# Kernel tuning notes

Hardware: AMD Instinct MI355X
Metric: run time of the kernel (lower is better)

## Reference

```python
import jax, jax.numpy as jnp
import numpy as np

N_NODES = 100000
N_EDGES = 1600000
IN_DIM = 64
OUT_DIM = 64
K_HEADS = 4
HEAD_DIM = OUT_DIM // K_HEADS


def setup_inputs() -> dict:
    key = jax.random.key(0)
    ks = jax.random.split(key, 12)
    x = jax.random.normal(ks[0], (N_NODES, IN_DIM), dtype=jnp.float32)
    edge_index = jax.random.randint(ks[1], (2, N_EDGES), 0, N_NODES, dtype=jnp.int64)
    edge_sign = jax.random.randint(ks[2], (N_EDGES,), 0, 2, dtype=jnp.int64)
    s = 1.0 / np.sqrt(IN_DIM)
    Wl_w = jax.random.uniform(ks[3], (OUT_DIM, IN_DIM), minval=-s, maxval=s, dtype=jnp.float32)
    Wl_b = jax.random.uniform(ks[4], (OUT_DIM,), minval=-s, maxval=s, dtype=jnp.float32)
    sign_tab = jax.random.normal(ks[5], (2, HEAD_DIM), dtype=jnp.float32)
    so = 1.0 / np.sqrt(OUT_DIM)
    Wh_w = jax.random.uniform(ks[6], (OUT_DIM, OUT_DIM), minval=-so, maxval=so, dtype=jnp.float32)
    Wh_b = jax.random.uniform(ks[7], (OUT_DIM,), minval=-so, maxval=so, dtype=jnp.float32)
    mlp_w1 = jax.random.uniform(ks[8], (OUT_DIM, OUT_DIM), minval=-so, maxval=so, dtype=jnp.float32)
    mlp_b1 = jax.random.uniform(ks[9], (OUT_DIM,), minval=-so, maxval=so, dtype=jnp.float32)
    mlp_w2 = jax.random.uniform(ks[10], (OUT_DIM, OUT_DIM), minval=-so, maxval=so, dtype=jnp.float32)
    mlp_b2 = jax.random.uniform(ks[11], (OUT_DIM,), minval=-so, maxval=so, dtype=jnp.float32)
    eps = jnp.zeros((1,), dtype=jnp.float32)
    return {"x": x, "edge_index": edge_index, "edge_sign": edge_sign,
            "Wl_w": Wl_w, "Wl_b": Wl_b, "sign_tab": sign_tab,
            "Wh_w": Wh_w, "Wh_b": Wh_b, "mlp_w1": mlp_w1, "mlp_b1": mlp_b1,
            "mlp_w2": mlp_w2, "mlp_b2": mlp_b2, "eps": eps}


def reference(x, edge_index, edge_sign, Wl_w, Wl_b, sign_tab, Wh_w, Wh_b,
              mlp_w1, mlp_b1, mlp_w2, mlp_b2, eps):
    N = x.shape[0]
    row, col = edge_index[0], edge_index[1]
    h = x @ Wl_w.T + Wl_b                              # [N, out_dim]
    hr = h.reshape(N, K_HEADS, HEAD_DIM)               # [N, K, hd]
    h_i = hr[row]                                      # [E, K, hd]
    h_j = hr[col]                                      # [E, K, hd]
    s_emb = sign_tab[edge_sign][:, None, :]            # [E, 1, hd]
    score = jnp.sum(h_i * h_j * s_emb, axis=-1)        # [E, K]
    # segment softmax over edges grouped by target node (row)
    mx = jax.ops.segment_max(score, row, num_segments=N)
    mx = jnp.where(jnp.isfinite(mx), mx, 0.0)          # empty segments -> 0
    ex = jnp.exp(score - mx[row])                      # [E, K]
    den = jax.ops.segment_sum(ex, row, num_segments=N)
    alpha = ex / (den[row] + 1e-16)                    # [E, K]
    # scatter-add weighted messages per head (vectorized over heads)
    msg = h_j * alpha[:, :, None]                      # [E, K, hd]
    aggr = jax.ops.segment_sum(msg, row, num_segments=N)  # [N, K, hd]
    m_l = aggr.reshape(N, OUT_DIM) @ Wh_w.T + Wh_b
    z = (1.0 + eps) * h + m_l
    hid = jax.nn.relu(z @ mlp_w1.T + mlp_b1)
    return hid @ mlp_w2.T + mlp_b2
```

## Files before the change

kernel.cpp:

```cpp
#include <hip/hip_runtime.h>

#define DIM 64
#define NBUCK 256
#define BSHIFT 9
#define BCAP 12288
#define CHUNK 4096

typedef __attribute__((ext_vector_type(4))) float f32x4;
typedef __attribute__((ext_vector_type(8))) short short8;
typedef __attribute__((ext_vector_type(4))) unsigned short ushort4v;

#define MFMA16(a, b, c) __builtin_amdgcn_mfma_f32_16x16x32_bf16(a, b, c, 0, 0, 0)

template <int CTRL>
__device__ __forceinline__ float qperm(float v) {
    return __int_as_float(__builtin_amdgcn_update_dpp(
        0, __float_as_int(v), CTRL, 0xF, 0xF, true));
}

__device__ __forceinline__ void cvt8(const float* f, short8& hi, short8& lo) {
#pragma unroll
    for (int e = 0; e < 8; ++e) {
        const unsigned u = __float_as_uint(f[e]);
        hi[e] = (short)(u >> 16);
        const float hf = __uint_as_float(u & 0xFFFF0000u);
        lo[e] = (short)(__float_as_uint(f[e] - hf) >> 16);
    }
}

__device__ __forceinline__ unsigned short bf16rne(float f) {
    const unsigned u = __float_as_uint(f);
    return (unsigned short)((u + 0x7FFFu + ((u >> 16) & 1u)) >> 16);
}

__global__ __launch_bounds__(256) void prep_kernel(
    const float* __restrict__ Wl, const float* __restrict__ Wh,
    const float* __restrict__ W1, const float* __restrict__ W2,
    short8* __restrict__ wf)
{
    const int tid = threadIdx.x;
    const int m = tid >> 6, l = tid & 63;
    const float* W = (m == 0) ? Wl : (m == 1) ? Wh : (m == 2) ? W1 : W2;
    const int o = l & 15;
    const int kg = (l >> 4) * 8;
#pragma unroll
    for (int t = 0; t < 4; ++t)
#pragma unroll
        for (int s = 0; s < 2; ++s) {
            float f[8];
#pragma unroll
            for (int e = 0; e < 8; ++e)
                f[e] = W[(o + 16 * t) * DIM + 32 * s + kg + e];
            short8 hi, lo;
            cvt8(f, hi, lo);
            const int base = (((m * 4 + t) * 2 + s) * 2);
            wf[(base + 0) * 64 + l] = hi;
            wf[(base + 1) * 64 + l] = lo;
        }
}

__global__ __launch_bounds__(256, 3) void gemm64_kernel(
    const float* __restrict__ x, const short8* __restrict__ wf,
    const float* __restrict__ bias, float* __restrict__ h,
    unsigned short* __restrict__ hb, int N)
{
    const int l = threadIdx.x & 63;
    const int gw = blockIdx.x * 4 + (threadIdx.x >> 6);
    const int nw = gridDim.x * 4;
    const int nstrips = (N + 15) >> 4;
    const int lr = l & 15, lk = (l >> 4) * 8, lrow4 = (l >> 4) * 4;

    short8 wh_[4][2], wl_[4][2];
#pragma unroll
    for (int t = 0; t < 4; ++t)
#pragma unroll
        for (int s = 0; s < 2; ++s) {
            wh_[t][s] = wf[(((0 * 4 + t) * 2 + s) * 2 + 0) * 64 + l];
            wl_[t][s] = wf[(((0 * 4 + t) * 2 + s) * 2 + 1) * 64 + l];
        }
    float b4[4];
#pragma unroll
    for (int t = 0; t < 4; ++t) b4[t] = bias[lr + 16 * t];

    for (int strip = gw; strip < nstrips; strip += nw) {
        const int rbase = strip * 16;
        const int arow = min(rbase + lr, N - 1);
        short8 ah[2], al[2];
#pragma unroll
        for (int s = 0; s < 2; ++s) {
            const float4 p0 = *reinterpret_cast<const float4*>(x + (size_t)arow * DIM + 32 * s + lk);
            const float4 p1 = *reinterpret_cast<const float4*>(x + (size_t)arow * DIM + 32 * s + lk + 4);
            float f[8] = {p0.x, p0.y, p0.z, p0.w, p1.x, p1.y, p1.z, p1.w};
            cvt8(f, ah[s], al[s]);
        }
        f32x4 acc[4];
#pragma unroll
        for (int t = 0; t < 4; ++t) acc[t] = (f32x4){b4[t], b4[t], b4[t], b4[t]};
#pragma unroll
        for (int s = 0; s < 2; ++s) {
#pragma unroll
            for (int t = 0; t < 4; ++t) acc[t] = MFMA16(ah[s], wh_[t][s], acc[t]);
#pragma unroll
            for (int t = 0; t < 4; ++t) acc[t] = MFMA16(ah[s], wl_[t][s], acc[t]);
#pragma unroll
            for (int t = 0; t < 4; ++t) acc[t] = MFMA16(al[s], wh_[t][s], acc[t]);
        }
#pragma unroll
        for (int t = 0; t < 4; ++t)
#pragma unroll
            for (int rg = 0; rg < 4; ++rg) {
                const int row = rbase + lrow4 + rg;
                if (row < N) {
                    h[(size_t)row * DIM + lr + 16 * t] = acc[t][rg];
                    hb[(size_t)row * DIM + lr + 16 * t] = bf16rne(acc[t][rg]);
                }
            }
    }
}

__global__ __launch_bounds__(256, 2) void tail_kernel(
    const float* __restrict__ aggr, const float* __restrict__ hres,
    const short8* __restrict__ wf,
    const float* __restrict__ bh, const float* __restrict__ b1,
    const float* __restrict__ b2, const float* __restrict__ eps,
    float* __restrict__ out, int N)
{
    __shared__ float zb[4][16 * 68];
    const int l = threadIdx.x & 63;
    const int w = threadIdx.x >> 6;
    const int gw = blockIdx.x * 4 + w;
    const int nw = gridDim.x * 4;
    const int nstrips = (N + 15) >> 4;
    const int lr = l & 15, lk = (l >> 4) * 8, lrow4 = (l >> 4) * 4;
    float* zw = zb[w];

    short8 whh[4][2], w1h[4][2], w2h[4][2];
#pragma unroll
    for (int t = 0; t < 4; ++t)
#pragma unroll
        for (int s = 0; s < 2; ++s) {
            whh[t][s] = wf[(((1 * 4 + t) * 2 + s) * 2 + 0) * 64 + l];
            w1h[t][s] = wf[(((2 * 4 + t) * 2 + s) * 2 + 0) * 64 + l];
            w2h[t][s] = wf[(((3 * 4 + t) * 2 + s) * 2 + 0) * 64 + l];
        }
    float bh4[4], b14[4], b24[4];
#pragma unroll
    for (int t = 0; t < 4; ++t) {
        bh4[t] = bh[lr + 16 * t];
        b14[t] = b1[lr + 16 * t];
        b24[t] = b2[lr + 16 * t];
    }
    const float escale = 1.0f + eps[0];

    for (int strip = gw; strip < nstrips; strip += nw) {
        const int rbase = strip * 16;

        float vh[4][4];
#pragma unroll
        for (int t = 0; t < 4; ++t)
#pragma unroll
            for (int rg = 0; rg < 4; ++rg)
                vh[t][rg] = hres[(size_t)min(rbase + lrow4 + rg, N - 1) * DIM + lr + 16 * t];

        const int arow = min(rbase + lr, N - 1);
        short8 ah[2], al[2];
#pragma unroll
        for (int s = 0; s < 2; ++s) {
            const float4 p0 = *reinterpret_cast<const float4*>(aggr + (size_t)arow * DIM + 32 * s + lk);
            const float4 p1 = *reinterpret_cast<const float4*>(aggr + (size_t)arow * DIM + 32 * s + lk + 4);
            float f[8] = {p0.x, p0.y, p0.z, p0.w, p1.x, p1.y, p1.z, p1.w};
            cvt8(f, ah[s], al[s]);
        }
        short8 lo_[4][2];
#pragma unroll
        for (int t = 0; t < 4; ++t)
#pragma unroll
            for (int s = 0; s < 2; ++s)
                lo_[t][s] = wf[(((1 * 4 + t) * 2 + s) * 2 + 1) * 64 + l];
        f32x4 acc[4];
#pragma unroll
        for (int t = 0; t < 4; ++t) acc[t] = (f32x4){bh4[t], bh4[t], bh4[t], bh4[t]};
#pragma unroll
        for (int s = 0; s < 2; ++s) {
#pragma unroll
            for (int t = 0; t < 4; ++t) acc[t] = MFMA16(ah[s], whh[t][s], acc[t]);
#pragma unroll
            for (int t = 0; t < 4; ++t) acc[t] = MFMA16(ah[s], lo_[t][s], acc[t]);
#pragma unroll
            for (int t = 0; t < 4; ++t) acc[t] = MFMA16(al[s], whh[t][s], acc[t]);
        }
#pragma unroll
        for (int t = 0; t < 4; ++t)
#pragma unroll
            for (int rg = 0; rg < 4; ++rg)
                zw[(lrow4 + rg) * 68 + lr + 16 * t] = fmaf(escale, vh[t][rg], acc[t][rg]);
        asm volatile("s_waitcnt lgkmcnt(0)" ::: "memory");

        short8 zh[2], zl[2];
#pragma unroll
        for (int s = 0; s < 2; ++s) {
            const float4 q0 = *reinterpret_cast<const float4*>(zw + lr * 68 + 32 * s + lk);
            const float4 q1 = *reinterpret_cast<const float4*>(zw + lr * 68 + 32 * s + lk + 4);
            float f[8] = {q0.x, q0.y, q0.z, q0.w, q1.x, q1.y, q1.z, q1.w};
            cvt8(f, zh[s], zl[s]);
        }
#pragma unroll
        for (int t = 0; t < 4; ++t)
#pragma unroll
            for (int s = 0; s < 2; ++s)
                lo_[t][s] = wf[(((2 * 4 + t) * 2 + s) * 2 + 1) * 64 + l];
#pragma unroll
        for (int t = 0; t < 4; ++t) acc[t] = (f32x4){b14[t], b14[t], b14[t], b14[t]};
#pragma unroll
        for (int s = 0; s < 2; ++s) {
#pragma unroll
            for (int t = 0; t < 4; ++t) acc[t] = MFMA16(zh[s], w1h[t][s], acc[t]);
#pragma unroll
            for (int t = 0; t < 4; ++t) acc[t] = MFMA16(zh[s], lo_[t][s], acc[t]);
#pragma unroll
            for (int t = 0; t < 4; ++t) acc[t] = MFMA16(zl[s], w1h[t][s], acc[t]);
        }
#pragma unroll
        for (int t = 0; t < 4; ++t)
#pragma unroll
            for (int rg = 0; rg < 4; ++rg)
                zw[(lrow4 + rg) * 68 + lr + 16 * t] = fmaxf(acc[t][rg], 0.f);
        asm volatile("s_waitcnt lgkmcnt(0)" ::: "memory");

        short8 hh[2], hl[2];
#pragma unroll
        for (int s = 0; s < 2; ++s) {
            const float4 q0 = *reinterpret_cast<const float4*>(zw + lr * 68 + 32 * s + lk);
            const float4 q1 = *reinterpret_cast<const float4*>(zw + lr * 68 + 32 * s + lk + 4);
            float f[8] = {q0.x, q0.y, q0.z, q0.w, q1.x, q1.y, q1.z, q1.w};
            cvt8(f, hh[s], hl[s]);
        }
#pragma unroll
        for (int t = 0; t < 4; ++t)
#pragma unroll
            for (int s = 0; s < 2; ++s)
                lo_[t][s] = wf[(((3 * 4 + t) * 2 + s) * 2 + 1) * 64 + l];
#pragma unroll
        for (int t = 0; t < 4; ++t) acc[t] = (f32x4){b24[t], b24[t], b24[t], b24[t]};
#pragma unroll
        for (int s = 0; s < 2; ++s) {
#pragma unroll
            for (int t = 0; t < 4; ++t) acc[t] = MFMA16(hh[s], w2h[t][s], acc[t]);
#pragma unroll
            for (int t = 0; t < 4; ++t) acc[t] = MFMA16(hh[s], lo_[t][s], acc[t]);
#pragma unroll
            for (int t = 0; t < 4; ++t) acc[t] = MFMA16(hl[s], w2h[t][s], acc[t]);
        }
#pragma unroll
        for (int t = 0; t < 4; ++t)
#pragma unroll
            for (int rg = 0; rg < 4; ++rg) {
                const int row = rbase + lrow4 + rg;
                if (row < N) out[(size_t)row * DIM + lr + 16 * t] = acc[t][rg];
            }
    }
}

__global__ __launch_bounds__(256) void zero256_kernel(int* __restrict__ p) {
    p[threadIdx.x] = 0;
}

__device__ __forceinline__ int wave_incl_scan(int v, int lane) {
#pragma unroll
    for (int off = 1; off < 64; off <<= 1) {
        int t = __shfl_up(v, (unsigned)off, 64);
        if (lane >= off) v += t;
    }
    return v;
}

__global__ __launch_bounds__(256) void bin_kernel(
    const int* __restrict__ ei, const int* __restrict__ sgn,
    int* __restrict__ bcursor, int* __restrict__ records, int E)
{
    const int tid = threadIdx.x;
    const int base = blockIdx.x * CHUNK;
    __shared__ int lcnt[NBUCK];
    __shared__ int lbase[NBUCK];
    lcnt[tid] = 0;
    __syncthreads();
    const int lim = min(CHUNK, E - base);
    for (int k = tid; k < lim; k += 256)
        atomicAdd(&lcnt[ei[base + k] >> BSHIFT], 1);
    __syncthreads();
    const int c = lcnt[tid];
    lbase[tid] = c ? atomicAdd(&bcursor[tid], c) : 0;
    lcnt[tid] = 0;
    __syncthreads();
    for (int k = tid; k < lim; k += 256) {
        const int e = base + k;
        const int r  = ei[e];
        const int cc = ei[E + e];
        const int s  = sgn[e];
        const int b  = r >> BSHIFT;
        const int idx = lbase[b] + atomicAdd(&lcnt[b], 1);
        if (idx < BCAP)
            records[b * BCAP + idx] = cc | (s << 17) | ((r & 511) << 18);
    }
}

__global__ __launch_bounds__(256) void scan256_kernel(
    const int* __restrict__ bcursor, int* __restrict__ csrb,
    int* __restrict__ offsets, int* __restrict__ edata, int N, int E)
{
    const int tid = threadIdx.x, lane = tid & 63, w = tid >> 6;
    const int v = min(bcursor[tid], BCAP);
    const int inc = wave_incl_scan(v, lane);
    __shared__ int wtot[4];
    if (lane == 63) wtot[w] = inc;
    __syncthreads();
    int add = 0;
#pragma unroll
    for (int i = 0; i < 4; ++i)
        if (i < w) add += wtot[i];
    csrb[tid] = add + inc - v;
    if (tid == 0) { offsets[N] = E; edata[E] = 0; }
}

__global__ __launch_bounds__(256) void build_kernel(
    const int* __restrict__ records, const int* __restrict__ bcursor,
    const int* __restrict__ csrb, int* __restrict__ offsets,
    int* __restrict__ edata, int N)
{
    const int b = blockIdx.x;
    const int tid = threadIdx.x, lane = tid & 63, w = tid >> 6;
    const int nbase = b << BSHIFT;
    const int nn = min(512, N - nbase);
    if (nn <= 0) return;
    const int cnt = min(bcursor[b], BCAP);
    const int base_csr = csrb[b];
    const int* rec = records + b * BCAP;

    __shared__ int ncnt[512];
    __shared__ int wtot[8];
    __shared__ int stag[BCAP];

    ncnt[tid] = 0; ncnt[256 + tid] = 0;
    __syncthreads();
    for (int i = tid; i < cnt; i += 256)
        atomicAdd(&ncnt[rec[i] >> 18], 1);
    __syncthreads();
    const int v0 = ncnt[tid], v1 = ncnt[256 + tid];
    const int i0 = wave_incl_scan(v0, lane);
    if (lane == 63) wtot[w] = i0;
    const int i1 = wave_incl_scan(v1, lane);
    if (lane == 63) wtot[4 + w] = i1;
    __syncthreads();
    int a0 = 0, a1 = 0;
#pragma unroll
    for (int i = 0; i < 4; ++i) {
        if (i < w) { a0 += wtot[i]; a1 += wtot[4 + i]; }
    }
    const int half = wtot[0] + wtot[1] + wtot[2] + wtot[3];
    const int e0 = a0 + i0 - v0;
    const int e1 = half + a1 + i1 - v1;
    if (tid < nn)       offsets[nbase + tid]       = base_csr + e0;
    if (256 + tid < nn) offsets[nbase + 256 + tid] = base_csr + e1;
    __syncthreads();
    ncnt[tid] = e0; ncnt[256 + tid] = e1;
    __syncthreads();
    for (int i = tid; i < cnt; i += 256) {
        const int rcd = rec[i];
        const int p = atomicAdd(&ncnt[rcd >> 18], 1);
        stag[p] = (rcd & 0x1FFFF) | (((rcd >> 17) & 1) << 20);
    }
    __syncthreads();
    for (int i = tid; i < cnt; i += 256)
        edata[base_csr + i] = stag[i];
}

__global__ __launch_bounds__(256) void attn_kernel(
    const float* __restrict__ h, const unsigned short* __restrict__ hb,
    const int* __restrict__ offsets, const int* __restrict__ edata,
    const float* __restrict__ sign_tab, float* __restrict__ aggr, int n)
{
    const int lane = threadIdx.x & 63;
    const int gl   = lane & 15;
    const int node = blockIdx.x * 16 + ((threadIdx.x >> 6) << 2) + (lane >> 4);
    const bool alive = node < n;

    int beg = 0, deg = 0;
    if (alive) {
        beg = offsets[node];
        deg = offsets[node + 1] - beg;
    }
    float4 hi = make_float4(0.f, 0.f, 0.f, 0.f);
    if (alive) hi = *reinterpret_cast<const float4*>(h + (size_t)node * DIM + gl * 4);

    const float4 s0 = *reinterpret_cast<const float4*>(sign_tab + (gl & 3) * 4);
    const float4 s1 = *reinterpret_cast<const float4*>(sign_tab + 16 + (gl & 3) * 4);
    const float4 hs0 = make_float4(hi.x * s0.x, hi.y * s0.y, hi.z * s0.z, hi.w * s0.w);
    const float4 hs1 = make_float4(hi.x * s1.x, hi.y * s1.y, hi.z * s1.z, hi.w * s1.w);

    const int degm1 = deg - 1;
    int maxdeg = max(deg, __shfl_xor(deg, 16, 64));
    maxdeg = max(maxdeg, __shfl_xor(maxdeg, 32, 64));

    float den = 0.f;
    float4 msg = make_float4(0.f, 0.f, 0.f, 0.f);

    for (int e = 0; e < maxdeg; e += 4) {
        int idx[4], pk[4];
#pragma unroll
        for (int u = 0; u < 4; ++u) idx[u] = max(0, min(e + u, degm1));
#pragma unroll
        for (int u = 0; u < 4; ++u) pk[u] = edata[beg + idx[u]];

        float4 hj[4];
#pragma unroll
        for (int u = 0; u < 4; ++u) {
            const int col = pk[u] & 0xFFFFF;
            const ushort4v v = *reinterpret_cast<const ushort4v*>(hb + (size_t)col * DIM + gl * 4);
            hj[u].x = __uint_as_float(((unsigned)v.x) << 16);
            hj[u].y = __uint_as_float(((unsigned)v.y) << 16);
            hj[u].z = __uint_as_float(((unsigned)v.z) << 16);
            hj[u].w = __uint_as_float(((unsigned)v.w) << 16);
        }

        float sc[4];
#pragma unroll
        for (int u = 0; u < 4; ++u) {
            const float4 wv = (pk[u] >> 20) ? hs1 : hs0;
            float s = wv.x * hj[u].x;
            s = fmaf(wv.y, hj[u].y, s);
            s = fmaf(wv.z, hj[u].z, s);
            s = fmaf(wv.w, hj[u].w, s);
            sc[u] = s;
        }
#pragma unroll
        for (int u = 0; u < 4; ++u) sc[u] += qperm<0xB1>(sc[u]);
#pragma unroll
        for (int u = 0; u < 4; ++u) sc[u] += qperm<0x4E>(sc[u]);

#pragma unroll
        for (int u = 0; u < 4; ++u) {
            const float ex = (e + u < deg) ? __expf(sc[u]) : 0.f;
            den += ex;
            msg.x = fmaf(ex, hj[u].x, msg.x);
            msg.y = fmaf(ex, hj[u].y, msg.y);
            msg.z = fmaf(ex, hj[u].z, msg.z);
            msg.w = fmaf(ex, hj[u].w, msg.w);
        }
    }

    if (alive) {
        const float inv = 1.0f / (den + 1e-16f);
        float4 o = make_float4(msg.x * inv, msg.y * inv, msg.z * inv, msg.w * inv);
        *reinterpret_cast<float4*>(aggr + (size_t)node * DIM + gl * 4) = o;
    }
}

extern "C" void kernel_launch(void* const* d_in, const int* in_sizes, int n_in,
                              void* d_out, int out_size, void* d_ws, size_t ws_size,
                              hipStream_t stream) {
    const float* x        = (const float*)d_in[0];
    const int*   ei       = (const int*)d_in[1];
    const int*   esign    = (const int*)d_in[2];
    const float* Wl_w     = (const float*)d_in[3];
    const float* Wl_b     = (const float*)d_in[4];
    const float* sign_tab = (const float*)d_in[5];
    const float* Wh_w     = (const float*)d_in[6];
    const float* Wh_b     = (const float*)d_in[7];
    const float* w1       = (const float*)d_in[8];
    const float* b1       = (const float*)d_in[9];
    const float* w2       = (const float*)d_in[10];
    const float* b2       = (const float*)d_in[11];
    const float* eps      = (const float*)d_in[12];
    float* out = (float*)d_out;

    const int N = in_sizes[0] / DIM;
    const int E = in_sizes[2];

    float* h       = (float*)d_ws;
    float* aggr    = h + (size_t)N * DIM;
    int*   records = (int*)aggr;
    int*   edata   = (int*)(aggr + (size_t)N * DIM);
    int*   bcursor = edata + (E + 1);
    int*   csrb    = bcursor + NBUCK;
    int*   offsets = csrb + NBUCK;
    short8* wf     = (short8*)(offsets + ((N + 1 + 3) & ~3));
    unsigned short* hb = (unsigned short*)d_out;

    prep_kernel<<<1, 256, 0, stream>>>(Wl_w, Wh_w, w1, w2, wf);

    gemm64_kernel<<<512, 256, 0, stream>>>(x, wf, Wl_b, h, hb, N);

    zero256_kernel<<<1, 256, 0, stream>>>(bcursor);
    bin_kernel<<<(E + CHUNK - 1) / CHUNK, 256, 0, stream>>>(ei, esign, bcursor, records, E);
    scan256_kernel<<<1, 256, 0, stream>>>(bcursor, csrb, offsets, edata, N, E);
    build_kernel<<<NBUCK, 256, 0, stream>>>(records, bcursor, csrb, offsets, edata, N);

    attn_kernel<<<(N + 15) / 16, 256, 0, stream>>>(h, hb, offsets, edata, sign_tab, aggr, N);

    tail_kernel<<<512, 256, 0, stream>>>(aggr, h, wf, Wh_b, b1, b2, eps, out, N);
}
```

Baseline: 132.9 us.

## Vectorize edge binning loads and streamline attention gather with packed math

The bin kernel now loads eight row, column and sign values per thread with int4 vector loads, using a smaller chunk so each block holds exactly 2048 edges. The attention kernel drops the per-edge index clamping by zero-padding edata past E, which lets the loop read beyond a node's degree safely. It also uses 32-bit address arithmetic, nontemporal edge loads and packed float2 math for the score and message accumulation. Together these cut instruction count and memory transactions, but they rely on the padding being large enough for the maximum over-read and on 32-bit offsets not overflowing.

```diff
diff --git a/kernel.cpp b/kernel.cpp
--- a/kernel.cpp
+++ b/kernel.cpp
@@ -4,11 +4,11 @@
 #define NBUCK 256
 #define BSHIFT 9
 #define BCAP 12288
-#define CHUNK 4096
+#define CHUNK 2048
 
 typedef __attribute__((ext_vector_type(4))) float f32x4;
+typedef __attribute__((ext_vector_type(2))) float f32x2v;
 typedef __attribute__((ext_vector_type(8))) short short8;
-typedef __attribute__((ext_vector_type(4))) unsigned short ushort4v;
 
 #define MFMA16(a, b, c) __builtin_amdgcn_mfma_f32_16x16x32_bf16(a, b, c, 0, 0, 0)
 
@@ -285,22 +285,57 @@
     lcnt[tid] = 0;
     __syncthreads();
     const int lim = min(CHUNK, E - base);
-    for (int k = tid; k < lim; k += 256)
-        atomicAdd(&lcnt[ei[base + k] >> BSHIFT], 1);
-    __syncthreads();
-    const int c = lcnt[tid];
-    lbase[tid] = c ? atomicAdd(&bcursor[tid], c) : 0;
-    lcnt[tid] = 0;
-    __syncthreads();
-    for (int k = tid; k < lim; k += 256) {
-        const int e = base + k;
-        const int r  = ei[e];
-        const int cc = ei[E + e];
-        const int s  = sgn[e];
-        const int b  = r >> BSHIFT;
-        const int idx = lbase[b] + atomicAdd(&lcnt[b], 1);
-        if (idx < BCAP)
-            records[b * BCAP + idx] = cc | (s << 17) | ((r & 511) << 18);
+    if (lim == CHUNK && (E & 3) == 0) {
+        int r[8];
+        {
+            const int4 a = *(reinterpret_cast<const int4*>(ei + base) + tid * 2);
+            const int4 b = *(reinterpret_cast<const int4*>(ei + base) + tid * 2 + 1);
+            r[0]=a.x; r[1]=a.y; r[2]=a.z; r[3]=a.w;
+            r[4]=b.x; r[5]=b.y; r[6]=b.z; r[7]=b.w;
+        }
+#pragma unroll
+        for (int i = 0; i < 8; ++i) atomicAdd(&lcnt[r[i] >> BSHIFT], 1);
+        __syncthreads();
+        const int c = lcnt[tid];
+        lbase[tid] = c ? atomicAdd(&bcursor[tid], c) : 0;
+        lcnt[tid] = 0;
+        __syncthreads();
+        int cc[8], ss[8];
+        {
+            const int4 a = *(reinterpret_cast<const int4*>(ei + E + base) + tid * 2);
+            const int4 b = *(reinterpret_cast<const int4*>(ei + E + base) + tid * 2 + 1);
+            cc[0]=a.x; cc[1]=a.y; cc[2]=a.z; cc[3]=a.w;
+            cc[4]=b.x; cc[5]=b.y; cc[6]=b.z; cc[7]=b.w;
+            const int4 s2 = *(reinterpret_cast<const int4*>(sgn + base) + tid * 2);
+            const int4 s3 = *(reinterpret_cast<const int4*>(sgn + base) + tid * 2 + 1);
+            ss[0]=s2.x; ss[1]=s2.y; ss[2]=s2.z; ss[3]=s2.w;
+            ss[4]=s3.x; ss[5]=s3.y; ss[6]=s3.z; ss[7]=s3.w;
+        }
+#pragma unroll
+        for (int i = 0; i < 8; ++i) {
+            const int bkt = r[i] >> BSHIFT;
+            const int idx = lbase[bkt] + atomicAdd(&lcnt[bkt], 1);
+            if (idx < BCAP)
+                records[bkt * BCAP + idx] = cc[i] | (ss[i] << 17) | ((r[i] & 511) << 18);
+        }
+    } else {
+        for (int k = tid; k < lim; k += 256)
+            atomicAdd(&lcnt[ei[base + k] >> BSHIFT], 1);
+        __syncthreads();
+        const int c = lcnt[tid];
+        lbase[tid] = c ? atomicAdd(&bcursor[tid], c) : 0;
+        lcnt[tid] = 0;
+        __syncthreads();
+        for (int k = tid; k < lim; k += 256) {
+            const int e = base + k;
+            const int rr = ei[e];
+            const int cc2 = ei[E + e];
+            const int s = sgn[e];
+            const int b = rr >> BSHIFT;
+            const int idx = lbase[b] + atomicAdd(&lcnt[b], 1);
+            if (idx < BCAP)
+                records[b * BCAP + idx] = cc2 | (s << 17) | ((rr & 511) << 18);
+        }
     }
 }
 
@@ -319,7 +354,9 @@
     for (int i = 0; i < 4; ++i)
         if (i < w) add += wtot[i];
     csrb[tid] = add + inc - v;
-    if (tid == 0) { offsets[N] = E; edata[E] = 0; }
+    if (tid == 0) offsets[N] = E;
+    edata[E + tid] = 0;
+    edata[E + 256 + tid] = 0;
 }
 
 __global__ __launch_bounds__(256) void build_kernel(
@@ -383,75 +420,62 @@
     const int gl   = lane & 15;
     const int node = blockIdx.x * 16 + ((threadIdx.x >> 6) << 2) + (lane >> 4);
     const bool alive = node < n;
-
-    int beg = 0, deg = 0;
-    if (alive) {
-        beg = offsets[node];
-        deg = offsets[node + 1] - beg;
-    }
-    float4 hi = make_float4(0.f, 0.f, 0.f, 0.f);
-    if (alive) hi = *reinterpret_cast<const float4*>(h + (size_t)node * DIM + gl * 4);
-
-    const float4 s0 = *reinterpret_cast<const float4*>(sign_tab + (gl & 3) * 4);
-    const float4 s1 = *reinterpret_cast<const float4*>(sign_tab + 16 + (gl & 3) * 4);
-    const float4 hs0 = make_float4(hi.x * s0.x, hi.y * s0.y, hi.z * s0.z, hi.w * s0.w);
-    const float4 hs1 = make_float4(hi.x * s1.x, hi.y * s1.y, hi.z * s1.z, hi.w * s1.w);
-
-    const int degm1 = deg - 1;
+    const int nidx = alive ? node : 0;
+
+    const int beg = offsets[nidx];
+    const int deg = offsets[nidx + 1] - beg;
+
+    const float4 hi = *reinterpret_cast<const float4*>(h + ((unsigned)nidx << 6) + (gl << 2));
+    const float4 s0 = *reinterpret_cast<const float4*>(sign_tab + ((gl & 3) << 2));
+    const float4 s1 = *reinterpret_cast<const float4*>(sign_tab + 16 + ((gl & 3) << 2));
+    const f32x2v hs0a = {hi.x * s0.x, hi.y * s0.y};
+    const f32x2v hs0b = {hi.z * s0.z, hi.w * s0.w};
+    const f32x2v hs1a = {hi.x * s1.x, hi.y * s1.y};
+    const f32x2v hs1b = {hi.z * s1.z, hi.w * s1.w};
+
     int maxdeg = max(deg, __shfl_xor(deg, 16, 64));
     maxdeg = max(maxdeg, __shfl_xor(maxdeg, 32, 64));
 
     float den = 0.f;
-    float4 msg = make_float4(0.f, 0.f, 0.f, 0.f);
+    f32x2v ma = {0.f, 0.f}, mb = {0.f, 0.f};
+    const unsigned glb = (unsigned)(gl << 3);
 
     for (int e = 0; e < maxdeg; e += 4) {
-        int idx[4], pk[4];
-#pragma unroll
-        for (int u = 0; u < 4; ++u) idx[u] = max(0, min(e + u, degm1));
-#pragma unroll
-        for (int u = 0; u < 4; ++u) pk[u] = edata[beg + idx[u]];
-
-        float4 hj[4];
+        int pk[4];
+#pragma unroll
+        for (int u = 0; u < 4; ++u)
+            pk[u] = __builtin_nontemporal_load(edata + (unsigned)(beg + e + u));
+        uint2 v[4];
 #pragma unroll
         for (int u = 0; u < 4; ++u) {
-            const int col = pk[u] & 0xFFFFF;
-            const ushort4v v = *reinterpret_cast<const ushort4v*>(hb + (size_t)col * DIM + gl * 4);
-            hj[u].x = __uint_as_float(((unsigned)v.x) << 16);
-            hj[u].y = __uint_as_float(((unsigned)v.y) << 16);
-            hj[u].z = __uint_as_float(((unsigned)v.z) << 16);
-            hj[u].w = __uint_as_float(((unsigned)v.w) << 16);
-        }
-
-        float sc[4];
+            const unsigned off = (((unsigned)pk[u] & 0x1FFFFu) << 7) + glb;
+            v[u] = *reinterpret_cast<const uint2*>(
+                reinterpret_cast<const char*>(hb) + off);
+        }
 #pragma unroll
         for (int u = 0; u < 4; ++u) {
-            const float4 wv = (pk[u] >> 20) ? hs1 : hs0;
-            float s = wv.x * hj[u].x;
-            s = fmaf(wv.y, hj[u].y, s);
-            s = fmaf(wv.z, hj[u].z, s);
-            s = fmaf(wv.w, hj[u].w, s);
-            sc[u] = s;
-        }
-#pragma unroll
-        for (int u = 0; u < 4; ++u) sc[u] += qperm<0xB1>(sc[u]);
-#pragma unroll
-        for (int u = 0; u < 4; ++u) sc[u] += qperm<0x4E>(sc[u]);
-
-#pragma unroll
-        for (int u = 0; u < 4; ++u) {
-            const float ex = (e + u < deg) ? __expf(sc[u]) : 0.f;
+            const f32x2v ha = {__uint_as_float(v[u].x << 16),
+                               __uint_as_float(v[u].x & 0xFFFF0000u)};
+            const f32x2v hc = {__uint_as_float(v[u].y << 16),
+                               __uint_as_float(v[u].y & 0xFFFF0000u)};
+            const bool sg = (pk[u] >> 20) & 1;
+            const f32x2v wa = sg ? hs1a : hs0a;
+            const f32x2v wb = sg ? hs1b : hs0b;
+            const f32x2v p = wa * ha + wb * hc;
+            float sc = p.x + p.y;
+            sc += qperm<0xB1>(sc);
+            sc += qperm<0x4E>(sc);
+            const float ex = (e + u < deg) ? __expf(sc) : 0.f;
             den += ex;
-            msg.x = fmaf(ex, hj[u].x, msg.x);
-            msg.y = fmaf(ex, hj[u].y, msg.y);
-            msg.z = fmaf(ex, hj[u].z, msg.z);
-            msg.w = fmaf(ex, hj[u].w, msg.w);
+            ma += ex * ha;
+            mb += ex * hc;
         }
     }
 
     if (alive) {
         const float inv = 1.0f / (den + 1e-16f);
-        float4 o = make_float4(msg.x * inv, msg.y * inv, msg.z * inv, msg.w * inv);
-        *reinterpret_cast<float4*>(aggr + (size_t)node * DIM + gl * 4) = o;
+        float4 o = make_float4(ma.x * inv, ma.y * inv, mb.x * inv, mb.y * inv);
+        *reinterpret_cast<float4*>(aggr + ((unsigned)node << 6) + (gl << 2)) = o;
     }
 }
 
@@ -480,7 +504,7 @@
     float* aggr    = h + (size_t)N * DIM;
     int*   records = (int*)aggr;
     int*   edata   = (int*)(aggr + (size_t)N * DIM);
-    int*   bcursor = edata + (E + 1);
+    int*   bcursor = edata + (E + 520);
     int*   csrb    = bcursor + NBUCK;
     int*   offsets = csrb + NBUCK;
     short8* wf     = (short8*)(offsets + ((N + 1 + 3) & ~3));
```

Measured after the change: 146.3 us. +10.1%, slower.
